# Performance work log

Hardware: AMD Instinct MI355X
Metric: run time of the kernel (lower is better)

## Reference

```python
import jax, jax.numpy as jnp
import numpy as np

EPS = 1e-6
WINDOW = 1024  # config.sliding_window; mask: causal AND (q_idx - kv_idx < WINDOW)


def rms_norm(x, w=None):
    y = x * jax.lax.rsqrt(jnp.mean(jnp.square(x), axis=-1, keepdims=True) + EPS)
    return y * w if w is not None else y


def rotate_half(x):
    x1, x2 = jnp.split(x, 2, axis=-1)
    return jnp.concatenate([-x2, x1], axis=-1)


def apply_rope(x, cos, sin):
    # x: [B,S,H,D], cos/sin: [B,S,D] -> unsqueeze head dim (rotary_dim == D, x_pass empty)
    cos = cos[:, :, None, :]
    sin = sin[:, :, None, :]
    return x * cos + rotate_half(x) * sin


def setup_inputs() -> dict:
    key = jax.random.key(0)
    ks = jax.random.split(key, 8)
    B, S, HID, NH, NKV, D = 1, 2048, 2560, 8, 4, 256
    scale = 0.02
    hidden_states = jax.random.normal(ks[0], (B, S, HID), dtype=jnp.float32)
    wq = jax.random.normal(ks[1], (HID, NH * D), dtype=jnp.float32) * scale
    wk = jax.random.normal(ks[2], (HID, NKV * D), dtype=jnp.float32) * scale
    wv = jax.random.normal(ks[3], (HID, NKV * D), dtype=jnp.float32) * scale
    wo = jax.random.normal(ks[4], (NH * D, HID), dtype=jnp.float32) * scale
    q_norm_w = jnp.ones((D,), dtype=jnp.float32)
    k_norm_w = jnp.ones((D,), dtype=jnp.float32)
    # standard RoPE tables, rotary_dim = head_dim
    pos = jnp.arange(S, dtype=jnp.float32)
    inv_freq = 1.0 / (10000.0 ** (jnp.arange(0, D, 2, dtype=jnp.float32) / D))
    freqs = pos[:, None] * inv_freq[None, :]           # [S, D/2]
    emb = jnp.concatenate([freqs, freqs], axis=-1)     # [S, D]
    cos = jnp.cos(emb)[None]                           # [1, S, D]
    sin = jnp.sin(emb)[None]
    return dict(hidden_states=hidden_states, cos=cos, sin=sin,
                wq=wq, wk=wk, wv=wv, wo=wo,
                q_norm_w=q_norm_w, k_norm_w=k_norm_w)


def reference(hidden_states, cos, sin, wq, wk, wv, wo, q_norm_w, k_norm_w):
    B, S, _ = hidden_states.shape
    D = q_norm_w.shape[0]
    # projections -> [B,S,H,D]
    q = (hidden_states @ wq).reshape(B, S, -1, D)
    k = (hidden_states @ wk).reshape(B, S, -1, D)
    v = (hidden_states @ wv).reshape(B, S, -1, D)
    # QK-norm then RoPE (v gets non-affine RMSNorm)
    q = apply_rope(rms_norm(q, q_norm_w), cos, sin)
    k = apply_rope(rms_norm(k, k_norm_w), cos, sin)
    v = rms_norm(v)
    NH, NKV = q.shape[2], k.shape[2]
    rep = NH // NKV  # GQA: repeat KV heads
    k = jnp.repeat(k, rep, axis=2)
    v = jnp.repeat(v, rep, axis=2)
    # attention with scale=1.0 (QK-norm replaces 1/sqrt(d))
    scores = jnp.einsum('bqhd,bkhd->bhqk', q, k)
    qi = jnp.arange(S)[:, None]
    ki = jnp.arange(S)[None, :]
    mask = (ki <= qi) & (qi - ki < WINDOW)  # causal sliding window
    scores = jnp.where(mask[None, None], scores, -jnp.inf)
    attn = jax.nn.softmax(scores, axis=-1)
    out = jnp.einsum('bhqk,bkhd->bqhd', attn, v).reshape(B, S, -1)
    return out @ wo
```

## Files before the change

kernel.cpp:

```cpp
#include <hip/hip_runtime.h>
#include <hip/hip_bf16.h>
#include <math.h>

#define S_LEN 2048
#define HID 2560
#define NH 8
#define NKV 4
#define HD 256
#define WINDOW 1024

typedef short short8 __attribute__((ext_vector_type(8)));
typedef short short4_t __attribute__((ext_vector_type(4)));
typedef float f32x4 __attribute__((ext_vector_type(4)));
typedef float float4_t __attribute__((ext_vector_type(4)));

__device__ __forceinline__ short bf16_rne(float x) {
  unsigned u = __float_as_uint(x);
  return (short)((u + 0x7FFFu + ((u >> 16) & 1u)) >> 16);
}
__device__ __forceinline__ void split2(float x, short &h, short &l) {
  unsigned u = __float_as_uint(x);
  unsigned hb = (u + 0x7FFFu + ((u >> 16) & 1u)) & 0xFFFF0000u;
  h = (short)(hb >> 16);
  float r = x - __uint_as_float(hb);
  l = bf16_rne(r);
}

__device__ __forceinline__ void gload16(const short* g, short* l) {
  __builtin_amdgcn_global_load_lds(
      (const __attribute__((address_space(1))) void*)g,
      (__attribute__((address_space(3))) void*)l, 16, 0, 0);
}

#define SWZ(g, r) ((((g) ^ ((r) & 7))) * 8)
template <int MODE>
__device__ __forceinline__ void gemm_body(
    const short* __restrict__ Ah, const short* __restrict__ Al,
    const short* __restrict__ Bh, const short* __restrict__ Bl,
    float* __restrict__ C, int Klen, int Kstr, int ldc, int m0, int n0, int tid,
    short (*__restrict__ Ahs)[64], short (*__restrict__ Als)[64],
    short (*__restrict__ Bhs)[64], short (*__restrict__ Bls)[64]) {
  constexpr bool USE_AL = (MODE & 1) != 0;
  constexpr bool USE_BL = (MODE & 2) != 0;
  const int wv = tid >> 6, lane = tid & 63;
  const int wm = (wv >> 1) * 32, wn = (wv & 1) * 64;
  const int quad = lane >> 4, col = lane & 15;
  const int lr = lane >> 3;
  const size_t lgofs = (size_t)(((lane & 7) ^ lr)) * 8;
  const size_t aBase = (size_t)(m0 + lr) * Kstr + lgofs;
  const size_t bBase = (size_t)(n0 + lr) * Kstr + lgofs;

  f32x4 acc[2][4];
#pragma unroll
  for (int i = 0; i < 2; i++)
#pragma unroll
    for (int j = 0; j < 4; j++) acc[i][j] = (f32x4){0.f, 0.f, 0.f, 0.f};

  for (int k0 = 0; k0 < Klen; k0 += 64) {
#pragma unroll
    for (int c = wv; c < 8; c += 4) {
      const size_t go = aBase + (size_t)c * 8 * Kstr + k0;
      gload16(Ah + go, &Ahs[c * 8][0]);
      if (USE_AL) gload16(Al + go, &Als[c * 8][0]);
    }
#pragma unroll
    for (int c = wv; c < 16; c += 4) {
      const size_t go = bBase + (size_t)c * 8 * Kstr + k0;
      gload16(Bh + go, &Bhs[c * 8][0]);
      if (USE_BL) gload16(Bl + go, &Bls[c * 8][0]);
    }
    __syncthreads();
#pragma unroll
    for (int ks = 0; ks < 2; ks++) {
      const int g = ks * 4 + quad;
      short8 afh[2], afl[2], bfh[4], bfl[4];
#pragma unroll
      for (int i = 0; i < 2; i++) {
        int ar = wm + i * 16 + col;
        afh[i] = *reinterpret_cast<const short8*>(&Ahs[ar][SWZ(g, ar)]);
        if (USE_AL)
          afl[i] = *reinterpret_cast<const short8*>(&Als[ar][SWZ(g, ar)]);
      }
#pragma unroll
      for (int j = 0; j < 4; j++) {
        int br = wn + j * 16 + col;
        bfh[j] = *reinterpret_cast<const short8*>(&Bhs[br][SWZ(g, br)]);
        if (USE_BL)
          bfl[j] = *reinterpret_cast<const short8*>(&Bls[br][SWZ(g, br)]);
      }
#pragma unroll
      for (int i = 0; i < 2; i++)
#pragma unroll
        for (int j = 0; j < 4; j++) {
          acc[i][j] = __builtin_amdgcn_mfma_f32_16x16x32_bf16(afh[i], bfh[j], acc[i][j], 0, 0, 0);
          if (USE_BL)
            acc[i][j] = __builtin_amdgcn_mfma_f32_16x16x32_bf16(afh[i], bfl[j], acc[i][j], 0, 0, 0);
          if (USE_AL)
            acc[i][j] = __builtin_amdgcn_mfma_f32_16x16x32_bf16(afl[i], bfh[j], acc[i][j], 0, 0, 0);
        }
    }
    __syncthreads();
  }
#pragma unroll
  for (int i = 0; i < 2; i++)
#pragma unroll
    for (int j = 0; j < 4; j++)
#pragma unroll
      for (int r = 0; r < 4; r++)
        C[(size_t)(m0 + wm + i * 16 + quad * 4 + r) * ldc + n0 + wn + j * 16 + col] =
            acc[i][j][r];
}

__global__ __launch_bounds__(256, 3)
void gemm_qkv(const short* __restrict__ Ah, const short* __restrict__ Al,
              const short* __restrict__ qkvTh, const short* __restrict__ qkvTl,
              float* __restrict__ Cqkv) {
  __shared__ short Ahs[64][64];
  __shared__ short Als[64][64];
  __shared__ short Bhs[128][64];
  __shared__ short Bls[128][64];
  const int b = blockIdx.x;
  if (b < 256) {
    gemm_body<2>(Ah, Al, qkvTh + (size_t)3072 * HID, qkvTl + (size_t)3072 * HID,
                 Cqkv + 3072, HID, HID, 4096, (b / 8) * 64, (b % 8) * 128,
                 threadIdx.x, Ahs, Als, Bhs, Bls);
  } else {
    const int t = b - 256;
    gemm_body<3>(Ah, Al, qkvTh, qkvTl, Cqkv, HID, HID, 4096, (t / 24) * 64,
                 (t % 24) * 128, threadIdx.x, Ahs, Als, Bhs, Bls);
  }
}

__global__ __launch_bounds__(256, 3)
void gemm_out(const short* __restrict__ ctxh, const short* __restrict__ woTh,
              const short* __restrict__ woTl, float* __restrict__ C1,
              float* __restrict__ C2) {
  __shared__ short Ahs[64][64];
  __shared__ short Als[1][64];
  __shared__ short Bhs[128][64];
  __shared__ short Bls[128][64];
  const int b = blockIdx.x;
  if (b < 640) {
    gemm_body<2>(ctxh, ctxh, woTh, woTl, C1, 1024, 2048, HID,
                 (b / 20) * 64, (b % 20) * 128, threadIdx.x, Ahs, Als, Bhs, Bls);
  } else {
    const int t = b - 640;
    gemm_body<2>(ctxh + 1024, ctxh + 1024, woTh + 1024, woTl + 1024, C2, 1024,
                 2048, HID, (t / 20) * 64, (t % 20) * 128, threadIdx.x, Ahs,
                 Als, Bhs, Bls);
  }
}

__global__ __launch_bounds__(256)
void addc_kernel(float* __restrict__ dst, const float* __restrict__ src) {
  const size_t i = ((size_t)blockIdx.x * 256 + threadIdx.x) * 2;
  float4_t a0 = reinterpret_cast<const float4_t*>(src)[i];
  float4_t a1 = reinterpret_cast<const float4_t*>(src)[i + 1];
  float4_t d0 = reinterpret_cast<const float4_t*>(dst)[i];
  float4_t d1 = reinterpret_cast<const float4_t*>(dst)[i + 1];
#pragma unroll
  for (int e = 0; e < 4; e++) { d0[e] += a0[e]; d1[e] += a1[e]; }
  reinterpret_cast<float4_t*>(dst)[i] = d0;
  reinterpret_cast<float4_t*>(dst)[i + 1] = d1;
}

__device__ __forceinline__ void wsplitT_body(const float* __restrict__ W,
                                             short* __restrict__ WTh,
                                             short* __restrict__ WTl,
                                             int KW, int NW, int n_ofs,
                                             int k0, int n0, int tid,
                                             float (*T)[65]) {
  const int r = tid >> 4, c4 = (tid & 15) * 4;
#pragma unroll
  for (int p = 0; p < 4; p++) {
    float4_t v = *reinterpret_cast<const float4_t*>(
        &W[(size_t)(k0 + r + p * 16) * NW + n0 + c4]);
#pragma unroll
    for (int e = 0; e < 4; e++) T[r + p * 16][c4 + e] = v[e];
  }
  __syncthreads();
  const int gk = tid & 7;
#pragma unroll
  for (int pass = 0; pass < 2; pass++) {
    const int n_loc = (tid >> 3) + pass * 32;
    short8 hv, lv;
#pragma unroll
    for (int e = 0; e < 8; e++) {
      short hh, ll;
      split2(T[gk * 8 + e][n_loc], hh, ll);
      hv[e] = hh; lv[e] = ll;
    }
    size_t base = (size_t)(n_ofs + n0 + n_loc) * KW + k0 + gk * 8;
    *reinterpret_cast<short8*>(WTh + base) = hv;
    *reinterpret_cast<short8*>(WTl + base) = lv;
  }
}

__global__ __launch_bounds__(256)
void prep_kernel(const float* __restrict__ hs, const float* __restrict__ wq,
                 const float* __restrict__ wk, const float* __restrict__ wv,
                 const float* __restrict__ wo, short* __restrict__ Ah,
                 short* __restrict__ Al, short* __restrict__ qkvTh,
                 short* __restrict__ qkvTl, short* __restrict__ woTh,
                 short* __restrict__ woTl) {
  __shared__ float T[64][65];
  const int bx = blockIdx.x;
  const int tid = threadIdx.x;
  if (bx < 5120) {
    const int i = bx * 256 + tid;
    float4_t v = reinterpret_cast<const float4_t*>(hs)[i];
    short4_t h, l;
#pragma unroll
    for (int e = 0; e < 4; e++) {
      short hh, ll;
      split2(v[e], hh, ll);
      h[e] = hh; l[e] = ll;
    }
    reinterpret_cast<short4_t*>(Ah)[i] = h;
    reinterpret_cast<short4_t*>(Al)[i] = l;
  } else if (bx < 6400) {
    const int local = bx - 5120;
    wsplitT_body(wq, qkvTh, qkvTl, HID, 2048, 0, (local % 40) * 64,
                 (local / 40) * 64, tid, T);
  } else if (bx < 7040) {
    const int local = bx - 6400;
    wsplitT_body(wk, qkvTh, qkvTl, HID, 1024, 2048, (local % 40) * 64,
                 (local / 40) * 64, tid, T);
  } else if (bx < 7680) {
    const int local = bx - 7040;
    wsplitT_body(wv, qkvTh, qkvTl, HID, 1024, 3072, (local % 40) * 64,
                 (local / 40) * 64, tid, T);
  } else {
    const int local = bx - 7680;
    wsplitT_body(wo, woTh, woTl, 2048, HID, 0, (local % 32) * 64,
                 (local / 32) * 64, tid, T);
  }
}

__global__ __launch_bounds__(256)
void norm_kernel(const float* __restrict__ Cqkv, const float* __restrict__ kw,
                 const float* __restrict__ cosb, const float* __restrict__ sinb,
                 short* __restrict__ kh, short* __restrict__ kl,
                 short* __restrict__ vtb) {
  const int unit = blockIdx.x * 4 + (threadIdx.x >> 6);
  const int u = unit & 7;
  const int sq = unit >> 3;
  const int t = threadIdx.x & 63;
  const int d = t * 4;
  const int colbase = (u < 4) ? 2048 + u * HD : 3072 + (u - 4) * HD;
  const float4_t x = *reinterpret_cast<const float4_t*>(
      &Cqkv[(size_t)sq * 4096 + colbase + d]);
  float v = x[0] * x[0] + x[1] * x[1] + x[2] * x[2] + x[3] * x[3];
#pragma unroll
  for (int off = 32; off; off >>= 1) v += __shfl_xor(v, off);
  const float scale = rsqrtf(v * (1.0f / HD) + 1e-6f);
  if (u < 4) {
    const float4_t w = *reinterpret_cast<const float4_t*>(kw + d);
    const float4_t cb = *reinterpret_cast<const float4_t*>(
        &cosb[(size_t)sq * HD + d]);
    const float4_t sb = *reinterpret_cast<const float4_t*>(
        &sinb[(size_t)sq * HD + d]);
    const float sgn = (t < 32) ? -1.f : 1.f;
    short4_t hv, lv;
#pragma unroll
    for (int e = 0; e < 4; e++) {
      const float n = x[e] * scale * w[e];
      const float other = __shfl_xor(n, 32);
      const float r = n * cb[e] + sgn * other * sb[e];
      short hh, ll;
      split2(r, hh, ll);
      hv[e] = hh; lv[e] = ll;
    }
    const size_t b = ((size_t)sq * NKV + u) * HD + d;
    *reinterpret_cast<short4_t*>(kh + b) = hv;
    *reinterpret_cast<short4_t*>(kl + b) = lv;
  } else {
    const int hh = u - 4;
#pragma unroll
    for (int e = 0; e < 4; e++)
      vtb[((size_t)hh * HD + d + e) * S_LEN + sq] = bf16_rne(x[e] * scale);
  }
}

#define KSW(g, r) (((g) ^ ((r) & 7)) * 8)
#define VSW(g, d) ((((g) + ((d) >> 1)) & 3) * 8)
__global__ __launch_bounds__(256, 2)
void flash_attn2(const float* __restrict__ qn, int qrs,
                 const float* __restrict__ qw, const float* __restrict__ cosb,
                 const float* __restrict__ sinb,
                 const short* __restrict__ kh, const short* __restrict__ kl,
                 const short* __restrict__ vtb, float* __restrict__ oA,
                 float* __restrict__ oB, float* __restrict__ mlA,
                 float* __restrict__ mlB) {
  __shared__ short Kh[32][256], Kl[32][256];
  __shared__ short Vb[256][32];
  __shared__ short Ps[64][32];
  const int qt = blockIdx.x, h = blockIdx.y, sp = blockIdx.z;
  const int kvh = h >> 1;
  const int q0 = qt * 64;
  const int tid = threadIdx.x;
  const int w = tid >> 6, lane = tid & 63;
  const int quad = lane >> 4, col = lane & 15;
  float* oOut = sp ? oB : oA;
  float* mlOut = sp ? mlB : mlA;
  short8 qh[8], ql[8];
  {
    const int sq = q0 + w * 16 + col;
    const float* qrow = qn + (size_t)sq * qrs + h * HD;
    float xq[8][8];
    float ssum = 0.f;
#pragma unroll
    for (int s8 = 0; s8 < 8; s8++) {
      const int d0 = s8 * 32 + quad * 8;
      float4_t a = *reinterpret_cast<const float4_t*>(qrow + d0);
      float4_t b = *reinterpret_cast<const float4_t*>(qrow + d0 + 4);
#pragma unroll
      for (int e = 0; e < 4; e++) {
        xq[s8][e] = a[e];
        xq[s8][4 + e] = b[e];
        ssum += a[e] * a[e] + b[e] * b[e];
      }
    }
    ssum += __shfl_xor(ssum, 16);
    ssum += __shfl_xor(ssum, 32);
    const float scale = rsqrtf(ssum * (1.0f / HD) + 1e-6f);
#pragma unroll
    for (int s8 = 0; s8 < 8; s8++) {
      const int d0 = s8 * 32 + quad * 8;
      float4_t w0 = *reinterpret_cast<const float4_t*>(qw + d0);
      float4_t w1 = *reinterpret_cast<const float4_t*>(qw + d0 + 4);
#pragma unroll
      for (int e = 0; e < 4; e++) {
        xq[s8][e] *= scale * w0[e];
        xq[s8][4 + e] *= scale * w1[e];
      }
    }
    const float* crow = cosb + (size_t)sq * HD;
    const float* srow = sinb + (size_t)sq * HD;
#pragma unroll
    for (int s8 = 0; s8 < 8; s8++) {
      const int d0 = s8 * 32 + quad * 8;
      float4_t c0 = *reinterpret_cast<const float4_t*>(crow + d0);
      float4_t c1 = *reinterpret_cast<const float4_t*>(crow + d0 + 4);
      float4_t s0 = *reinterpret_cast<const float4_t*>(srow + d0);
      float4_t s1 = *reinterpret_cast<const float4_t*>(srow + d0 + 4);
      const float sgn = (s8 < 4) ? -1.f : 1.f;
      const int pp = s8 ^ 4;
#pragma unroll
      for (int e = 0; e < 4; e++) {
        short hh, ll;
        split2(xq[s8][e] * c0[e] + sgn * xq[pp][e] * s0[e], hh, ll);
        qh[s8][e] = hh; ql[s8][e] = ll;
        split2(xq[s8][4 + e] * c1[e] + sgn * xq[pp][4 + e] * s1[e], hh, ll);
        qh[s8][4 + e] = hh; ql[s8][4 + e] = ll;
      }
    }
  }
  f32x4 o[16];
#pragma unroll
  for (int i = 0; i < 16; i++) o[i] = (f32x4){0.f, 0.f, 0.f, 0.f};
  float m_r[4] = {-INFINITY, -INFINITY, -INFINITY, -INFINITY};
  float l_r[4] = {0.f, 0.f, 0.f, 0.f};
  const int lo_t = (q0 > 1023) ? ((q0 - 1023) >> 5) : 0;
  const int hi_t = (q0 + 63) >> 5;
  const int halfn = (hi_t - lo_t + 2) >> 1;
  const int t0 = sp ? (lo_t + halfn) : lo_t;
  const int t1 = sp ? hi_t : (lo_t + halfn - 1);
  for (int kt = t0; kt <= t1; kt++) {
    const int kt0 = kt << 5;
    __syncthreads();
#pragma unroll
    for (int i = 0; i < 4; i++) {
      int idx = tid + i * 256;
      int row = idx >> 5, g = idx & 31;
      size_t gofs = ((size_t)(kt0 + row) * NKV + kvh) * HD + g * 8;
      *reinterpret_cast<short8*>(&Kh[row][KSW(g, row)]) =
          *reinterpret_cast<const short8*>(kh + gofs);
      *reinterpret_cast<short8*>(&Kl[row][KSW(g, row)]) =
          *reinterpret_cast<const short8*>(kl + gofs);
    }
#pragma unroll
    for (int i = 0; i < 4; i++) {
      int idx = tid + i * 256;
      int d = idx >> 2, g = idx & 3;
      *reinterpret_cast<short8*>(&Vb[d][VSW(g, d)]) =
          *reinterpret_cast<const short8*>(
              vtb + ((size_t)kvh * HD + d) * S_LEN + kt0 + g * 8);
    }
    __syncthreads();
    f32x4 sc[2];
    sc[0] = (f32x4){0.f, 0.f, 0.f, 0.f};
    sc[1] = (f32x4){0.f, 0.f, 0.f, 0.f};
#pragma unroll
    for (int s8 = 0; s8 < 8; s8++) {
#pragma unroll
      for (int nt = 0; nt < 2; nt++) {
        const int br = nt * 16 + col;
        const short8 bh = *reinterpret_cast<const short8*>(
            &Kh[br][KSW(s8 * 4 + quad, br)]);
        const short8 bl = *reinterpret_cast<const short8*>(
            &Kl[br][KSW(s8 * 4 + quad, br)]);
        sc[nt] = __builtin_amdgcn_mfma_f32_16x16x32_bf16(qh[s8], bh, sc[nt], 0, 0, 0);
        sc[nt] = __builtin_amdgcn_mfma_f32_16x16x32_bf16(qh[s8], bl, sc[nt], 0, 0, 0);
        sc[nt] = __builtin_amdgcn_mfma_f32_16x16x32_bf16(ql[s8], bh, sc[nt], 0, 0, 0);
      }
    }
#pragma unroll
    for (int r = 0; r < 4; r++) {
      const int q_abs = q0 + w * 16 + quad * 4 + r;
      const int prow = w * 16 + quad * 4 + r;
#pragma unroll
      for (int nt = 0; nt < 2; nt++) {
        int k_abs = kt0 + nt * 16 + col;
        bool valid = (k_abs <= q_abs) && (q_abs - k_abs < WINDOW);
        if (!valid) sc[nt][r] = -INFINITY;
      }
      float mx = fmaxf(sc[0][r], sc[1][r]);
      mx = fmaxf(mx, __shfl_xor(mx, 1));
      mx = fmaxf(mx, __shfl_xor(mx, 2));
      mx = fmaxf(mx, __shfl_xor(mx, 4));
      mx = fmaxf(mx, __shfl_xor(mx, 8));
      if (!__all(mx <= m_r[r] + 8.f)) {
        const float mn = fmaxf(m_r[r], mx);
        const float alpha = (mn == -INFINITY) ? 1.f : __expf(m_r[r] - mn);
        m_r[r] = mn;
        l_r[r] *= alpha;
#pragma unroll
        for (int nt2 = 0; nt2 < 16; nt2++) o[nt2][r] *= alpha;
      }
      float rsum = 0.f;
#pragma unroll
      for (int nt = 0; nt < 2; nt++) {
        float s = sc[nt][r];
        float e = (s == -INFINITY) ? 0.f : __expf(s - m_r[r]);
        rsum += e;
        int ge = nt * 2 + (col >> 3);
        Ps[prow][VSW(ge, prow) + (col & 7)] = bf16_rne(e);
      }
      rsum += __shfl_xor(rsum, 1);
      rsum += __shfl_xor(rsum, 2);
      rsum += __shfl_xor(rsum, 4);
      rsum += __shfl_xor(rsum, 8);
      l_r[r] += rsum;
    }
    __syncthreads();
    {
      const int prow = w * 16 + col;
      const short8 pa = *reinterpret_cast<const short8*>(&Ps[prow][VSW(quad, prow)]);
#pragma unroll
      for (int nt = 0; nt < 16; nt++) {
        const int vr = nt * 16 + col;
        const short8 vb = *reinterpret_cast<const short8*>(&Vb[vr][VSW(quad, vr)]);
        o[nt] = __builtin_amdgcn_mfma_f32_16x16x32_bf16(pa, vb, o[nt], 0, 0, 0);
      }
    }
  }
#pragma unroll
  for (int r = 0; r < 4; r++) {
    const int row = q0 + w * 16 + quad * 4 + r;
    const size_t base = ((size_t)row * NH + h) * HD;
#pragma unroll
    for (int nt = 0; nt < 16; nt++) oOut[base + nt * 16 + col] = o[nt][r];
    if (col == 0) {
      mlOut[((size_t)row * NH + h) * 2] = m_r[r];
      mlOut[((size_t)row * NH + h) * 2 + 1] = l_r[r];
    }
  }
}

__global__ __launch_bounds__(256)
void combine_kernel(const float* __restrict__ oA, const float* __restrict__ oB,
                    const float* __restrict__ mlA, const float* __restrict__ mlB,
                    short* __restrict__ ctxh) {
  const int unit = blockIdx.x * 8 + (threadIdx.x >> 5);
  const int t = threadIdx.x & 31;
  const float mA = mlA[(size_t)unit * 2], lA = mlA[(size_t)unit * 2 + 1];
  const float mB = mlB[(size_t)unit * 2], lB = mlB[(size_t)unit * 2 + 1];
  const float m = fmaxf(mA, mB);
  const float eA = (mA == -INFINITY) ? 0.f : __expf(mA - m);
  const float eB = (mB == -INFINITY) ? 0.f : __expf(mB - m);
  const float inv = 1.0f / (eA * lA + eB * lB);
  const size_t b = (size_t)unit * HD + t * 8;
  const float4_t a0 = *reinterpret_cast<const float4_t*>(oA + b);
  const float4_t a1 = *reinterpret_cast<const float4_t*>(oA + b + 4);
  const float4_t b0 = *reinterpret_cast<const float4_t*>(oB + b);
  const float4_t b1 = *reinterpret_cast<const float4_t*>(oB + b + 4);
  short8 out;
#pragma unroll
  for (int e = 0; e < 4; e++) {
    out[e] = bf16_rne((eA * a0[e] + eB * b0[e]) * inv);
    out[4 + e] = bf16_rne((eA * a1[e] + eB * b1[e]) * inv);
  }
  *reinterpret_cast<short8*>(ctxh + b) = out;
}

extern "C" void kernel_launch(void* const* d_in, const int* in_sizes, int n_in,
                              void* d_out, int out_size, void* d_ws, size_t ws_size,
                              hipStream_t stream) {
  const float* hs   = (const float*)d_in[0];
  const float* cosb = (const float*)d_in[1];
  const float* sinb = (const float*)d_in[2];
  const float* wq   = (const float*)d_in[3];
  const float* wk   = (const float*)d_in[4];
  const float* wv   = (const float*)d_in[5];
  const float* wo   = (const float*)d_in[6];
  const float* qw   = (const float*)d_in[7];
  const float* kw   = (const float*)d_in[8];
  dim3 blk(256);

  const size_t szAh   = (size_t)S_LEN * HID * 2;
  const size_t szQKVT = (size_t)4096 * HID * 2;
  const size_t szWoT  = (size_t)HID * 2048 * 2;
  const size_t szCqkv = (size_t)S_LEN * 4096 * 4;
  const size_t szKh   = (size_t)S_LEN * NKV * HD * 2;
  const size_t szMl   = (size_t)S_LEN * NH * 2 * 4;

  char* p = (char*)d_ws + 256;
  short* Ah    = (short*)p;  p += szAh;
  short* Al    = (short*)p;  p += szAh;
  short* qkvTh = (short*)p;  p += szQKVT;
  short* qkvTl = (short*)p;  p += szQKVT;
  short* woTh  = (short*)p;  p += szWoT;
  short* woTl  = (short*)p;  p += szWoT;
  float* Cqkv  = (float*)p;  p += szCqkv;
  short* kh    = (short*)p;  p += szKh;
  short* kl    = (short*)p;  p += szKh;
  short* vtb   = (short*)p;  p += szKh;
  float* mlA   = (float*)p;  p += szMl;
  float* mlB   = (float*)p;  p += szMl;
  float* oA    = (float*)Ah;
  float* oB    = (float*)d_out;
  short* ctxh  = qkvTh;
  float* C2    = Cqkv;

  prep_kernel<<<8960, blk, 0, stream>>>(hs, wq, wk, wv, wo, Ah, Al, qkvTh,
                                        qkvTl, woTh, woTl);
  gemm_qkv<<<1024, blk, 0, stream>>>(Ah, Al, qkvTh, qkvTl, Cqkv);
  norm_kernel<<<4096, blk, 0, stream>>>(Cqkv, kw, cosb, sinb, kh, kl, vtb);
  flash_attn2<<<dim3(S_LEN / 64, NH, 2), blk, 0, stream>>>(
      Cqkv, 4096, qw, cosb, sinb, kh, kl, vtb, oA, oB, mlA, mlB);
  combine_kernel<<<2048, blk, 0, stream>>>(oA, oB, mlA, mlB, ctxh);
  gemm_out<<<1280, blk, 0, stream>>>(ctxh, woTh, woTl, (float*)d_out, C2);
  addc_kernel<<<2560, blk, 0, stream>>>((float*)d_out, C2);
}
```

Before: 422.1 us.

## Replace split-K output GEMM with 128x128 tile kernel and drop add pass

Rewrites the output projection as a single kernel with 128x128 tiles over the full K=2048, so it no longer splits K into two halves that write separate buffers and then need an extra add kernel. This removes one launch and the read-modify-write traffic of the partial-sum buffer, and larger tiles improve operand reuse. In exchange only 320 blocks are launched, which may underfill the GPU, and each block does a longer serial K loop with more registers for the accumulators.

Result: no change. 418.5 us (-0.9%).

```diff
diff --git a/kernel.cpp b/kernel.cpp
--- a/kernel.cpp
+++ b/kernel.cpp
@@ -132,36 +132,69 @@
 }
 
 __global__ __launch_bounds__(256, 3)
-void gemm_out(const short* __restrict__ ctxh, const short* __restrict__ woTh,
-              const short* __restrict__ woTl, float* __restrict__ C1,
-              float* __restrict__ C2) {
-  __shared__ short Ahs[64][64];
-  __shared__ short Als[1][64];
+void gemm_out128(const short* __restrict__ ctxh, const short* __restrict__ woTh,
+                 const short* __restrict__ woTl, float* __restrict__ C) {
+  __shared__ short Ahs[128][64];
   __shared__ short Bhs[128][64];
   __shared__ short Bls[128][64];
-  const int b = blockIdx.x;
-  if (b < 640) {
-    gemm_body<2>(ctxh, ctxh, woTh, woTl, C1, 1024, 2048, HID,
-                 (b / 20) * 64, (b % 20) * 128, threadIdx.x, Ahs, Als, Bhs, Bls);
-  } else {
-    const int t = b - 640;
-    gemm_body<2>(ctxh + 1024, ctxh + 1024, woTh + 1024, woTl + 1024, C2, 1024,
-                 2048, HID, (t / 20) * 64, (t % 20) * 128, threadIdx.x, Ahs,
-                 Als, Bhs, Bls);
-  }
-}
-
-__global__ __launch_bounds__(256)
-void addc_kernel(float* __restrict__ dst, const float* __restrict__ src) {
-  const size_t i = ((size_t)blockIdx.x * 256 + threadIdx.x) * 2;
-  float4_t a0 = reinterpret_cast<const float4_t*>(src)[i];
-  float4_t a1 = reinterpret_cast<const float4_t*>(src)[i + 1];
-  float4_t d0 = reinterpret_cast<const float4_t*>(dst)[i];
-  float4_t d1 = reinterpret_cast<const float4_t*>(dst)[i + 1];
-#pragma unroll
-  for (int e = 0; e < 4; e++) { d0[e] += a0[e]; d1[e] += a1[e]; }
-  reinterpret_cast<float4_t*>(dst)[i] = d0;
-  reinterpret_cast<float4_t*>(dst)[i + 1] = d1;
+  const int tid = threadIdx.x;
+  const int wv = tid >> 6, lane = tid & 63;
+  const int wm = (wv >> 1) * 64, wn = (wv & 1) * 64;
+  const int quad = lane >> 4, col = lane & 15;
+  const int m0 = (blockIdx.x / 20) * 128, n0 = (blockIdx.x % 20) * 128;
+  const int lr = lane >> 3;
+  const size_t lgofs = (size_t)(((lane & 7) ^ lr)) * 8;
+  const size_t aBase = (size_t)(m0 + lr) * 2048 + lgofs;
+  const size_t bBase = (size_t)(n0 + lr) * 2048 + lgofs;
+
+  f32x4 acc[4][4];
+#pragma unroll
+  for (int i = 0; i < 4; i++)
+#pragma unroll
+    for (int j = 0; j < 4; j++) acc[i][j] = (f32x4){0.f, 0.f, 0.f, 0.f};
+
+  for (int k0 = 0; k0 < 2048; k0 += 64) {
+#pragma unroll
+    for (int c = wv; c < 16; c += 4) {
+      gload16(ctxh + aBase + (size_t)c * 8 * 2048 + k0, &Ahs[c * 8][0]);
+      const size_t gb = bBase + (size_t)c * 8 * 2048 + k0;
+      gload16(woTh + gb, &Bhs[c * 8][0]);
+      gload16(woTl + gb, &Bls[c * 8][0]);
+    }
+    __syncthreads();
+#pragma unroll
+    for (int ks = 0; ks < 2; ks++) {
+      const int g = ks * 4 + quad;
+      short8 afh[4], bfh[4], bfl[4];
+#pragma unroll
+      for (int i = 0; i < 4; i++) {
+        int ar = wm + i * 16 + col;
+        afh[i] = *reinterpret_cast<const short8*>(&Ahs[ar][SWZ(g, ar)]);
+      }
+#pragma unroll
+      for (int j = 0; j < 4; j++) {
+        int br = wn + j * 16 + col;
+        bfh[j] = *reinterpret_cast<const short8*>(&Bhs[br][SWZ(g, br)]);
+        bfl[j] = *reinterpret_cast<const short8*>(&Bls[br][SWZ(g, br)]);
+      }
+#pragma unroll
+      for (int i = 0; i < 4; i++)
+#pragma unroll
+        for (int j = 0; j < 4; j++) {
+          acc[i][j] = __builtin_amdgcn_mfma_f32_16x16x32_bf16(afh[i], bfh[j], acc[i][j], 0, 0, 0);
+          acc[i][j] = __builtin_amdgcn_mfma_f32_16x16x32_bf16(afh[i], bfl[j], acc[i][j], 0, 0, 0);
+        }
+    }
+    __syncthreads();
+  }
+#pragma unroll
+  for (int i = 0; i < 4; i++)
+#pragma unroll
+    for (int j = 0; j < 4; j++)
+#pragma unroll
+      for (int r = 0; r < 4; r++)
+        C[(size_t)(m0 + wm + i * 16 + quad * 4 + r) * HID + n0 + wn + j * 16 + col] =
+            acc[i][j][r];
 }
 
 __device__ __forceinline__ void wsplitT_body(const float* __restrict__ W,
@@ -531,7 +564,6 @@
   float* oA    = (float*)Ah;
   float* oB    = (float*)d_out;
   short* ctxh  = qkvTh;
-  float* C2    = Cqkv;
 
   prep_kernel<<<8960, blk, 0, stream>>>(hs, wq, wk, wv, wo, Ah, Al, qkvTh,
                                         qkvTl, woTh, woTl);
@@ -540,6 +572,5 @@
   flash_attn2<<<dim3(S_LEN / 64, NH, 2), blk, 0, stream>>>(
       Cqkv, 4096, qw, cosb, sinb, kh, kl, vtb, oA, oB, mlA, mlB);
   combine_kernel<<<2048, blk, 0, stream>>>(oA, oB, mlA, mlB, ctxh);
-  gemm_out<<<1280, blk, 0, stream>>>(ctxh, woTh, woTl, (float*)d_out, C2);
-  addc_kernel<<<2560, blk, 0, stream>>>((float*)d_out, C2);
-}
+  gemm_out128<<<320, blk, 0, stream>>>(ctxh, woTh, woTl, (float*)d_out);
+}
```
